# Kernel tuning notes

Hardware: AMD Instinct MI355X
Metric: run time of the kernel (lower is better)

Reference implementation:

```python
import jax, jax.numpy as jnp
import numpy as np

N_NODES = 100000
N_EDGES = 3200000
IN_C, HID_C, OUT_C = 128, 16, 5
NEG_SLOPE = 0.2


def setup_inputs() -> dict:
    key = jax.random.key(0)
    ks = jax.random.split(key, 12)
    x = jax.random.normal(ks[0], (N_NODES, IN_C), dtype=jnp.float32)
    edge_index = jax.random.randint(ks[1], (2, N_EDGES), 0, N_NODES, dtype=jnp.int64)
    # GATConv layer 1 params (heads=1)
    s1 = 1.0 / np.sqrt(IN_C)
    W1 = jax.random.uniform(ks[2], (IN_C, HID_C), jnp.float32, -s1, s1)
    att_src1 = jax.random.uniform(ks[3], (HID_C,), jnp.float32, -1.0, 1.0) * s1
    att_dst1 = jax.random.uniform(ks[4], (HID_C,), jnp.float32, -1.0, 1.0) * s1
    b1 = jnp.zeros((HID_C,), jnp.float32)
    # GATConv layer 2 params
    s2 = 1.0 / np.sqrt(HID_C)
    W2 = jax.random.uniform(ks[5], (HID_C, OUT_C), jnp.float32, -s2, s2)
    att_src2 = jax.random.uniform(ks[6], (OUT_C,), jnp.float32, -1.0, 1.0) * s2
    att_dst2 = jax.random.uniform(ks[7], (OUT_C,), jnp.float32, -1.0, 1.0) * s2
    b2 = jnp.zeros((OUT_C,), jnp.float32)
    return {"x": x, "edge_index": edge_index,
            "W1": W1, "att_src1": att_src1, "att_dst1": att_dst1, "b1": b1,
            "W2": W2, "att_src2": att_src2, "att_dst2": att_dst2, "b2": b2}


def gat_layer(x, src, dst, W, att_src, att_dst, bias, n_nodes):
    # project: [N, C_out]
    h = x @ W
    a_src = h @ att_src  # [N]
    a_dst = h @ att_dst  # [N]
    e = a_src[src] + a_dst[dst]            # [E]
    e = jax.nn.leaky_relu(e, NEG_SLOPE)
    # per-destination-node softmax over incoming edges (stable)
    m = jax.ops.segment_max(e, dst, num_segments=n_nodes)
    ex = jnp.exp(e - m[dst])
    denom = jax.ops.segment_sum(ex, dst, num_segments=n_nodes)
    alpha = ex / (denom[dst] + 1e-16)      # [E]
    # weighted scatter-aggregate of source features
    out = jax.ops.segment_sum(h[src] * alpha[:, None], dst, num_segments=n_nodes)
    return out + bias


def reference(x, edge_index, W1, att_src1, att_dst1, b1, W2, att_src2, att_dst2, b2):
    n = x.shape[0]
    loops = jnp.arange(n, dtype=edge_index.dtype)
    src = jnp.concatenate([edge_index[0], loops])  # add_self_loops=True
    dst = jnp.concatenate([edge_index[1], loops])
    h = gat_layer(x, src, dst, W1, att_src1, att_dst1, b1, n)
    h = jax.nn.relu(h)
    h = gat_layer(h, src, dst, W2, att_src2, att_dst2, b2, n)
    return jax.nn.log_softmax(h, axis=1)
```

## Files before the change

kernel.cpp:

```cpp
#include <hip/hip_runtime.h>
#include <hip/hip_fp16.h>

#define N_NODES 100000
#define N_EDGES 3200000
#define E_TOT   (N_EDGES + N_NODES)
#define IN_C 128
#define HID  16
#define OUTC 5
#define NEG_SLOPE 0.2f

#define NBKT 391
#define CAP  9216
#define P1_TILE 8192
#define P1_GRID ((E_TOT + P1_TILE - 1) / P1_TILE)

__device__ __forceinline__ float pk_half2(float a, float b) {
    __half2 h = __halves2half2(__float2half(a), __float2half(b));
    return *(float*)&h;
}
__device__ __forceinline__ float2 unpk_half2(float v) {
    return __half22float2(*(__half2*)&v);
}

__global__ void zero_gcnt_k(int* __restrict__ gcnt) {
    int i = blockIdx.x * blockDim.x + threadIdx.x;
    if (i < NBKT) gcnt[i] = 0;
}

__global__ __launch_bounds__(256) void part_k(const int* __restrict__ ei,
                                              int* __restrict__ gcnt,
                                              unsigned* __restrict__ pairs) {
    __shared__ unsigned vbuf[P1_TILE];
    __shared__ unsigned short bbuf[P1_TILE];
    __shared__ int hist[NBKT];
    __shared__ int cur[NBKT];
    int t = threadIdx.x;
    for (int i = t; i < NBKT; i += 256) hist[i] = 0;
    __syncthreads();
    int base = blockIdx.x * P1_TILE;
    int lim = E_TOT - base; if (lim > P1_TILE) lim = P1_TILE;
    for (int i = t; i < lim; i += 256) {
        int e = base + i;
        int s, d;
        if (e < N_EDGES) { s = ei[e]; d = ei[N_EDGES + e]; }
        else             { s = e - N_EDGES; d = s; }
        int b = d >> 8;
        vbuf[i] = ((unsigned)s << 8) | (unsigned)(d & 255);
        bbuf[i] = (unsigned short)b;
        atomicAdd(&hist[b], 1);
    }
    __syncthreads();
    for (int i = t; i < NBKT; i += 256) {
        int h = hist[i];
        cur[i] = h ? atomicAdd(&gcnt[i], h) : 0;
    }
    __syncthreads();
    for (int i = t; i < lim; i += 256) {
        int b = bbuf[i];
        int p = atomicAdd(&cur[b], 1);
        if (p >= 0 && p < CAP) pairs[(size_t)b * CAP + p] = vbuf[i];
    }
}

__global__ void scan_gcnt_k(const int* __restrict__ gcnt, int* __restrict__ cbase) {
    __shared__ int s[512];
    int t = threadIdx.x;
    int v = (t < NBKT) ? gcnt[t] : 0;
    s[t] = v; __syncthreads();
    for (int off = 1; off < 512; off <<= 1) {
        int x = (t >= off) ? s[t - off] : 0;
        __syncthreads();
        s[t] += x;
        __syncthreads();
    }
    if (t < NBKT) cbase[t] = s[t] - v;
}

__global__ __launch_bounds__(256) void build_k(const unsigned* __restrict__ pairs,
                                               const int* __restrict__ gcnt,
                                               const int* __restrict__ cbase,
                                               int* __restrict__ csr,
                                               int* __restrict__ row_start,
                                               int* __restrict__ cnt) {
    __shared__ int c[256], s[256], cur[256];
    int t = threadIdx.x;
    int b = blockIdx.x;
    c[t] = 0;
    __syncthreads();
    int tot = gcnt[b];
    if (tot > CAP) tot = CAP;
    size_t pbase = (size_t)b * CAP;
    for (int i = t; i < tot; i += 256) atomicAdd(&c[pairs[pbase + i] & 255u], 1);
    __syncthreads();
    int v0 = c[t];
    s[t] = v0; __syncthreads();
    for (int off = 1; off < 256; off <<= 1) {
        int x = (t >= off) ? s[t - off] : 0;
        __syncthreads();
        s[t] += x;
        __syncthreads();
    }
    int excl = s[t] - v0;
    int gbase = cbase[b];
    int node = (b << 8) + t;
    if (node < N_NODES) { row_start[node] = gbase + excl; cnt[node] = v0; }
    cur[t] = gbase + excl;
    __syncthreads();
    for (int i = t; i < tot; i += 256) {
        unsigned v = pairs[pbase + i];
        int pos = atomicAdd(&cur[v & 255u], 1);
        csr[pos] = (int)(v >> 8);
    }
}

__global__ void proj1_k(const float* __restrict__ x, const float* __restrict__ W1,
                        const float* __restrict__ att_s, const float* __restrict__ att_d,
                        __half* __restrict__ h1f, float* __restrict__ a_src,
                        float* __restrict__ a_dst) {
    __shared__ float sW[IN_C * HID];
    __shared__ float sX[16 * IN_C];
    __shared__ float sH[16 * HID];
    int t = threadIdx.x;
    for (int i = t; i < IN_C * HID; i += 256) sW[i] = W1[i];
    int node0 = blockIdx.x * 16;
    for (int i = t; i < 16 * IN_C; i += 256) {
        int r = i >> 7, c = i & 127;
        int node = node0 + r;
        sX[i] = (node < N_NODES) ? x[(size_t)node * IN_C + c] : 0.0f;
    }
    __syncthreads();
    int r = t >> 4, c = t & 15;
    int node = node0 + r;
    float acc = 0.0f;
    #pragma unroll 8
    for (int k = 0; k < IN_C; ++k) acc += sX[r * IN_C + k] * sW[k * HID + c];
    sH[r * HID + c] = acc;
    if (node < N_NODES) h1f[(size_t)node * HID + c] = __float2half(acc);
    __syncthreads();
    if (c == 0 && node < N_NODES) {
        float s = 0.0f, d = 0.0f;
        #pragma unroll
        for (int k = 0; k < HID; ++k) {
            float hv = sH[r * HID + k];
            s += hv * att_s[k];
            d += hv * att_d[k];
        }
        a_src[node] = s;
        a_dst[node] = d;
    }
}

__global__ __launch_bounds__(256) void gat1_k(
    const int* __restrict__ csr, const int* __restrict__ row_start,
    const int* __restrict__ cnt, const __half* __restrict__ h1f,
    const float* __restrict__ a_src1, const float* __restrict__ a_dst1,
    const float* __restrict__ b1, const float* __restrict__ W2,
    const float* __restrict__ as2, const float* __restrict__ ad2,
    float4* __restrict__ h2p, float* __restrict__ a_dst2) {
    __shared__ float sW2[HID * OUTC];
    __shared__ float sB1[HID];
    __shared__ float sAs[OUTC], sAd[OUTC];
    int t = threadIdx.x;
    if (t < HID * OUTC) sW2[t] = W2[t];
    if (t < HID) sB1[t] = b1[t];
    if (t < OUTC) { sAs[t] = as2[t]; sAd[t] = ad2[t]; }
    __syncthreads();

    int node = (blockIdx.x * 256 + t) >> 4;
    int lane = t & 15;
    int start = row_start[node];
    int len   = cnt[node];
    float ad  = a_dst1[node];

    float acc[HID];
    #pragma unroll
    for (int c = 0; c < HID; ++c) acc[c] = 0.0f;
    float accd = 0.0f;
    for (int it = lane; it < len; it += 16) {
        int s = csr[start + it];
        float v = a_src1[s] + ad;
        v = (v > 0.0f) ? v : NEG_SLOPE * v;
        float ex = __expf(v);
        accd += ex;
        const float4* hp = (const float4*)(h1f + (size_t)s * HID);
        float4 r0 = hp[0], r1 = hp[1];
        float2 f0 = unpk_half2(r0.x), f1 = unpk_half2(r0.y);
        float2 f2 = unpk_half2(r0.z), f3 = unpk_half2(r0.w);
        float2 f4 = unpk_half2(r1.x), f5 = unpk_half2(r1.y);
        float2 f6 = unpk_half2(r1.z), f7 = unpk_half2(r1.w);
        acc[0]  += ex * f0.x; acc[1]  += ex * f0.y;
        acc[2]  += ex * f1.x; acc[3]  += ex * f1.y;
        acc[4]  += ex * f2.x; acc[5]  += ex * f2.y;
        acc[6]  += ex * f3.x; acc[7]  += ex * f3.y;
        acc[8]  += ex * f4.x; acc[9]  += ex * f4.y;
        acc[10] += ex * f5.x; acc[11] += ex * f5.y;
        acc[12] += ex * f6.x; acc[13] += ex * f6.y;
        acc[14] += ex * f7.x; acc[15] += ex * f7.y;
    }
    #pragma unroll
    for (int off = 8; off; off >>= 1) {
        accd += __shfl_xor(accd, off);
        #pragma unroll
        for (int c = 0; c < HID; ++c) acc[c] += __shfl_xor(acc[c], off);
    }
    if (lane == 0) {
        float inv = 1.0f / (accd + 1e-16f);
        float g[HID];
        #pragma unroll
        for (int k = 0; k < HID; ++k) g[k] = fmaxf(acc[k] * inv + sB1[k], 0.0f);
        float h2[OUTC];
        #pragma unroll
        for (int c = 0; c < OUTC; ++c) {
            float a = 0.0f;
            #pragma unroll
            for (int k = 0; k < HID; ++k) a += g[k] * sW2[k * OUTC + c];
            h2[c] = a;
        }
        float s2 = 0.0f, d2 = 0.0f;
        #pragma unroll
        for (int c = 0; c < OUTC; ++c) { s2 += h2[c] * sAs[c]; d2 += h2[c] * sAd[c]; }
        a_dst2[node] = d2;
        float4 r;
        r.x = s2;
        r.y = pk_half2(h2[0], h2[1]);
        r.z = pk_half2(h2[2], h2[3]);
        r.w = pk_half2(h2[4], 0.0f);
        h2p[node] = r;
    }
}

__global__ __launch_bounds__(256) void gat2_k(
    const int* __restrict__ csr, const int* __restrict__ row_start,
    const int* __restrict__ cnt, const float4* __restrict__ h2p,
    const float* __restrict__ a_dst2, const float* __restrict__ b2,
    float* __restrict__ out) {
    __shared__ float sB2[OUTC];
    int t = threadIdx.x;
    if (t < OUTC) sB2[t] = b2[t];
    __syncthreads();

    int node = (blockIdx.x * 256 + t) >> 4;
    int lane = t & 15;
    int start = row_start[node];
    int len   = cnt[node];
    float ad  = a_dst2[node];

    float acc[OUTC];
    #pragma unroll
    for (int c = 0; c < OUTC; ++c) acc[c] = 0.0f;
    float accd = 0.0f;
    for (int it = lane; it < len; it += 16) {
        int s = csr[start + it];
        float4 r = h2p[s];
        float v = r.x + ad;
        v = (v > 0.0f) ? v : NEG_SLOPE * v;
        float ex = __expf(v);
        accd += ex;
        float2 f01 = unpk_half2(r.y);
        float2 f23 = unpk_half2(r.z);
        float2 f4_ = unpk_half2(r.w);
        acc[0] += ex * f01.x; acc[1] += ex * f01.y;
        acc[2] += ex * f23.x; acc[3] += ex * f23.y;
        acc[4] += ex * f4_.x;
    }
    #pragma unroll
    for (int off = 8; off; off >>= 1) {
        accd += __shfl_xor(accd, off);
        #pragma unroll
        for (int c = 0; c < OUTC; ++c) acc[c] += __shfl_xor(acc[c], off);
    }
    if (lane == 0) {
        float inv = 1.0f / (accd + 1e-16f);
        float val[OUTC];
        float mx = -3.4e38f;
        #pragma unroll
        for (int c = 0; c < OUTC; ++c) {
            val[c] = acc[c] * inv + sB2[c];
            mx = fmaxf(mx, val[c]);
        }
        float se = 0.0f;
        #pragma unroll
        for (int c = 0; c < OUTC; ++c) se += __expf(val[c] - mx);
        float lse = logf(se) + mx;
        #pragma unroll
        for (int c = 0; c < OUTC; ++c)
            out[(size_t)node * OUTC + c] = val[c] - lse;
    }
}

extern "C" void kernel_launch(void* const* d_in, const int* in_sizes, int n_in,
                              void* d_out, int out_size, void* d_ws, size_t ws_size,
                              hipStream_t stream) {
    const float* x    = (const float*)d_in[0];
    const int*   ei   = (const int*)d_in[1];
    const float* W1   = (const float*)d_in[2];
    const float* as1  = (const float*)d_in[3];
    const float* ad1  = (const float*)d_in[4];
    const float* b1   = (const float*)d_in[5];
    const float* W2   = (const float*)d_in[6];
    const float* as2  = (const float*)d_in[7];
    const float* ad2  = (const float*)d_in[8];
    const float* b2   = (const float*)d_in[9];
    float* out = (float*)d_out;

    char* wsb = (char*)d_ws;
    unsigned* pairs = (unsigned*)wsb;
    __half* h1f     = (__half*)wsb;
    float4* h2p     = (float4*)(wsb + 3200000);
    float*  asrc1   = (float*)(wsb + 4800000);
    float*  adst1   = asrc1 + N_NODES;
    float*  adst2   = adst1 + N_NODES;
    int* csr       = (int*)(wsb + (size_t)NBKT * CAP * 4);
    int* cnt       = csr + E_TOT;
    int* row_start = cnt + N_NODES;
    int* gcnt      = row_start + N_NODES;
    int* cbase     = gcnt + NBKT;

    const int B = 256;
    const int gW = (N_NODES * 16) / B;

    zero_gcnt_k<<<(NBKT + B - 1) / B, B, 0, stream>>>(gcnt);
    part_k<<<P1_GRID, B, 0, stream>>>(ei, gcnt, pairs);
    scan_gcnt_k<<<1, 512, 0, stream>>>(gcnt, cbase);
    build_k<<<NBKT, B, 0, stream>>>(pairs, gcnt, cbase, csr, row_start, cnt);

    proj1_k<<<(N_NODES + 15) / 16, 256, 0, stream>>>(x, W1, as1, ad1, h1f, asrc1, adst1);
    gat1_k<<<gW, B, 0, stream>>>(csr, row_start, cnt, h1f, asrc1, adst1, b1,
                                 W2, as2, ad2, h2p, adst2);
    gat2_k<<<gW, B, 0, stream>>>(csr, row_start, cnt, h2p, adst2, b2, out);
}
```

Measured before the change: 274.3 us.

## Use 4 lanes per node in GAT aggregation, finer buckets, two-pass partition

```diff
diff --git a/kernel.cpp b/kernel.cpp
--- a/kernel.cpp
+++ b/kernel.cpp
@@ -9,10 +9,10 @@
 #define OUTC 5
 #define NEG_SLOPE 0.2f
 
-#define NBKT 391
-#define CAP  9216
-#define P1_TILE 8192
-#define P1_GRID ((E_TOT + P1_TILE - 1) / P1_TILE)
+#define NBKT 782
+#define CAP  4608
+#define P_TILE 8192
+#define P_GRID ((E_TOT + P_TILE - 1) / P_TILE)
 
 __device__ __forceinline__ float pk_half2(float a, float b) {
     __half2 h = __halves2half2(__float2half(a), __float2half(b));
@@ -27,47 +27,44 @@
     if (i < NBKT) gcnt[i] = 0;
 }
 
-__global__ __launch_bounds__(256) void part_k(const int* __restrict__ ei,
+__global__ __launch_bounds__(512) void part_k(const int* __restrict__ ei,
                                               int* __restrict__ gcnt,
                                               unsigned* __restrict__ pairs) {
-    __shared__ unsigned vbuf[P1_TILE];
-    __shared__ unsigned short bbuf[P1_TILE];
     __shared__ int hist[NBKT];
     __shared__ int cur[NBKT];
     int t = threadIdx.x;
-    for (int i = t; i < NBKT; i += 256) hist[i] = 0;
-    __syncthreads();
-    int base = blockIdx.x * P1_TILE;
-    int lim = E_TOT - base; if (lim > P1_TILE) lim = P1_TILE;
-    for (int i = t; i < lim; i += 256) {
+    for (int i = t; i < NBKT; i += 512) hist[i] = 0;
+    __syncthreads();
+    int base = blockIdx.x * P_TILE;
+    int lim = E_TOT - base; if (lim > P_TILE) lim = P_TILE;
+    for (int i = t; i < lim; i += 512) {
+        int e = base + i;
+        int d = (e < N_EDGES) ? ei[N_EDGES + e] : (e - N_EDGES);
+        atomicAdd(&hist[d >> 7], 1);
+    }
+    __syncthreads();
+    for (int i = t; i < NBKT; i += 512) {
+        int h = hist[i];
+        cur[i] = h ? atomicAdd(&gcnt[i], h) : 0;
+    }
+    __syncthreads();
+    for (int i = t; i < lim; i += 512) {
         int e = base + i;
         int s, d;
         if (e < N_EDGES) { s = ei[e]; d = ei[N_EDGES + e]; }
         else             { s = e - N_EDGES; d = s; }
-        int b = d >> 8;
-        vbuf[i] = ((unsigned)s << 8) | (unsigned)(d & 255);
-        bbuf[i] = (unsigned short)b;
-        atomicAdd(&hist[b], 1);
-    }
-    __syncthreads();
-    for (int i = t; i < NBKT; i += 256) {
-        int h = hist[i];
-        cur[i] = h ? atomicAdd(&gcnt[i], h) : 0;
-    }
-    __syncthreads();
-    for (int i = t; i < lim; i += 256) {
-        int b = bbuf[i];
+        int b = d >> 7;
         int p = atomicAdd(&cur[b], 1);
-        if (p >= 0 && p < CAP) pairs[(size_t)b * CAP + p] = vbuf[i];
+        if (p >= 0 && p < CAP) pairs[(size_t)b * CAP + p] = ((unsigned)s << 7) | (unsigned)(d & 127);
     }
 }
 
 __global__ void scan_gcnt_k(const int* __restrict__ gcnt, int* __restrict__ cbase) {
-    __shared__ int s[512];
+    __shared__ int s[1024];
     int t = threadIdx.x;
     int v = (t < NBKT) ? gcnt[t] : 0;
     s[t] = v; __syncthreads();
-    for (int off = 1; off < 512; off <<= 1) {
+    for (int off = 1; off < 1024; off <<= 1) {
         int x = (t >= off) ? s[t - off] : 0;
         __syncthreads();
         s[t] += x;
@@ -82,34 +79,36 @@
                                                int* __restrict__ csr,
                                                int* __restrict__ row_start,
                                                int* __restrict__ cnt) {
-    __shared__ int c[256], s[256], cur[256];
+    __shared__ int c[128], s[128], cur[128];
     int t = threadIdx.x;
     int b = blockIdx.x;
-    c[t] = 0;
+    if (t < 128) c[t] = 0;
     __syncthreads();
     int tot = gcnt[b];
     if (tot > CAP) tot = CAP;
     size_t pbase = (size_t)b * CAP;
-    for (int i = t; i < tot; i += 256) atomicAdd(&c[pairs[pbase + i] & 255u], 1);
-    __syncthreads();
-    int v0 = c[t];
-    s[t] = v0; __syncthreads();
-    for (int off = 1; off < 256; off <<= 1) {
-        int x = (t >= off) ? s[t - off] : 0;
+    for (int i = t; i < tot; i += 256) atomicAdd(&c[pairs[pbase + i] & 127u], 1);
+    __syncthreads();
+    if (t < 128) { s[t] = c[t]; }
+    __syncthreads();
+    for (int off = 1; off < 128; off <<= 1) {
+        int x = (t < 128 && t >= off) ? s[t - off] : 0;
         __syncthreads();
-        s[t] += x;
+        if (t < 128) s[t] += x;
         __syncthreads();
     }
-    int excl = s[t] - v0;
     int gbase = cbase[b];
-    int node = (b << 8) + t;
-    if (node < N_NODES) { row_start[node] = gbase + excl; cnt[node] = v0; }
-    cur[t] = gbase + excl;
+    if (t < 128) {
+        int excl = s[t] - c[t];
+        int node = (b << 7) + t;
+        if (node < N_NODES) { row_start[node] = gbase + excl; cnt[node] = c[t]; }
+        cur[t] = gbase + excl;
+    }
     __syncthreads();
     for (int i = t; i < tot; i += 256) {
         unsigned v = pairs[pbase + i];
-        int pos = atomicAdd(&cur[v & 255u], 1);
-        csr[pos] = (int)(v >> 8);
+        int pos = atomicAdd(&cur[v & 127u], 1);
+        csr[pos] = (int)(v >> 7);
     }
 }
 
@@ -121,12 +120,16 @@
     __shared__ float sX[16 * IN_C];
     __shared__ float sH[16 * HID];
     int t = threadIdx.x;
-    for (int i = t; i < IN_C * HID; i += 256) sW[i] = W1[i];
+    const float4* W4 = (const float4*)W1;
+    for (int i = t; i < IN_C * HID / 4; i += 256) ((float4*)sW)[i] = W4[i];
     int node0 = blockIdx.x * 16;
-    for (int i = t; i < 16 * IN_C; i += 256) {
-        int r = i >> 7, c = i & 127;
+    const float4* x4 = (const float4*)x;
+    for (int i = t; i < 16 * IN_C / 4; i += 256) {
+        int r = i >> 5, c4 = i & 31;
         int node = node0 + r;
-        sX[i] = (node < N_NODES) ? x[(size_t)node * IN_C + c] : 0.0f;
+        float4 v = make_float4(0.f, 0.f, 0.f, 0.f);
+        if (node < N_NODES) v = x4[(size_t)node * 32 + c4];
+        *((float4*)&sX[r * IN_C + c4 * 4]) = v;
     }
     __syncthreads();
     int r = t >> 4, c = t & 15;
@@ -166,8 +169,9 @@
     if (t < OUTC) { sAs[t] = as2[t]; sAd[t] = ad2[t]; }
     __syncthreads();
 
-    int node = (blockIdx.x * 256 + t) >> 4;
-    int lane = t & 15;
+    int node = (blockIdx.x * 256 + t) >> 2;
+    if (node >= N_NODES) return;
+    int lane = t & 3;
     int start = row_start[node];
     int len   = cnt[node];
     float ad  = a_dst1[node];
@@ -176,7 +180,7 @@
     #pragma unroll
     for (int c = 0; c < HID; ++c) acc[c] = 0.0f;
     float accd = 0.0f;
-    for (int it = lane; it < len; it += 16) {
+    for (int it = lane; it < len; it += 4) {
         int s = csr[start + it];
         float v = a_src1[s] + ad;
         v = (v > 0.0f) ? v : NEG_SLOPE * v;
@@ -198,7 +202,7 @@
         acc[14] += ex * f7.x; acc[15] += ex * f7.y;
     }
     #pragma unroll
-    for (int off = 8; off; off >>= 1) {
+    for (int off = 2; off; off >>= 1) {
         accd += __shfl_xor(accd, off);
         #pragma unroll
         for (int c = 0; c < HID; ++c) acc[c] += __shfl_xor(acc[c], off);
@@ -239,8 +243,9 @@
     if (t < OUTC) sB2[t] = b2[t];
     __syncthreads();
 
-    int node = (blockIdx.x * 256 + t) >> 4;
-    int lane = t & 15;
+    int node = (blockIdx.x * 256 + t) >> 2;
+    if (node >= N_NODES) return;
+    int lane = t & 3;
     int start = row_start[node];
     int len   = cnt[node];
     float ad  = a_dst2[node];
@@ -249,7 +254,7 @@
     #pragma unroll
     for (int c = 0; c < OUTC; ++c) acc[c] = 0.0f;
     float accd = 0.0f;
-    for (int it = lane; it < len; it += 16) {
+    for (int it = lane; it < len; it += 4) {
         int s = csr[start + it];
         float4 r = h2p[s];
         float v = r.x + ad;
@@ -264,7 +269,7 @@
         acc[4] += ex * f4_.x;
     }
     #pragma unroll
-    for (int off = 8; off; off >>= 1) {
+    for (int off = 2; off; off >>= 1) {
         accd += __shfl_xor(accd, off);
         #pragma unroll
         for (int c = 0; c < OUTC; ++c) acc[c] += __shfl_xor(acc[c], off);
@@ -317,11 +322,11 @@
     int* cbase     = gcnt + NBKT;
 
     const int B = 256;
-    const int gW = (N_NODES * 16) / B;
+    const int gW = (N_NODES * 4 + B - 1) / B;
 
     zero_gcnt_k<<<(NBKT + B - 1) / B, B, 0, stream>>>(gcnt);
-    part_k<<<P1_GRID, B, 0, stream>>>(ei, gcnt, pairs);
-    scan_gcnt_k<<<1, 512, 0, stream>>>(gcnt, cbase);
+    part_k<<<P_GRID, 512, 0, stream>>>(ei, gcnt, pairs);
+    scan_gcnt_k<<<1, 1024, 0, stream>>>(gcnt, cbase);
     build_k<<<NBKT, B, 0, stream>>>(pairs, gcnt, cbase, csr, row_start, cnt);
 
     proj1_k<<<(N_NODES + 15) / 16, 256, 0, stream>>>(x, W1, as1, ad1, h1f, asrc1, adst1);
```

New measurement: 270.3 us. About the same (-1.5%).
